# Kernel tuning notes

Hardware: AMD Instinct MI355X
Metric: run time of the kernel (lower is better)

The kernel has to match this reference:

```python
import jax, jax.numpy as jnp
import numpy as np

N = 100000       # nodes
E = 3200000      # edges (avg degree 32)
IN = 64          # in_channels
HID = 32         # hidden_channels
HEADS = 2
OUT = 1
EPS = 1e-5       # LayerNorm eps
SLOPE = 0.2      # LeakyReLU negative slope (PyG default)


def setup_inputs() -> dict:
    key = jax.random.key(0)
    ks = jax.random.split(key, 18)
    def nrm(k, shape, scale=0.1):
        return jax.random.normal(k, shape, dtype=jnp.float32) * scale
    return {
        "x": jax.random.normal(ks[0], (N, IN), dtype=jnp.float32),
        "edge_index": jax.random.randint(ks[1], (2, E), 0, N, dtype=jnp.int64),
        # GATConv layer 1 (concat=True)
        "W1": nrm(ks[2], (IN, HEADS * HID)),
        "a_src1": nrm(ks[3], (HEADS, HID)),
        "a_dst1": nrm(ks[4], (HEADS, HID)),
        "b1": jnp.zeros((HEADS * HID,), jnp.float32),
        "ln1_g": jnp.ones((HEADS * HID,), jnp.float32),
        "ln1_b": jnp.zeros((HEADS * HID,), jnp.float32),
        # GATConv layer 2 (heads=1, concat=False)
        "W2": nrm(ks[5], (HEADS * HID, HID)),
        "a_src2": nrm(ks[6], (1, HID)),
        "a_dst2": nrm(ks[7], (1, HID)),
        "b2": jnp.zeros((HID,), jnp.float32),
        "ln2_g": jnp.ones((HID,), jnp.float32),
        "ln2_b": jnp.zeros((HID,), jnp.float32),
        # output Linear
        "Wout": nrm(ks[8], (HID, OUT)),
        "bout": jnp.zeros((OUT,), jnp.float32),
    }


def layer_norm(x, g, b):
    mu = jnp.mean(x, axis=-1, keepdims=True)
    var = jnp.mean(jnp.square(x - mu), axis=-1, keepdims=True)
    return (x - mu) * jax.lax.rsqrt(var + EPS) * g + b


def gat_conv(x, edge_index, W, a_src, a_dst, bias, heads, ch, concat):
    """PyG GATConv (add_self_loops=True, bias=True), eval mode (no dropout)."""
    n = x.shape[0]
    loop = jnp.arange(n, dtype=edge_index.dtype)
    src = jnp.concatenate([edge_index[0], loop])   # [E+N]
    dst = jnp.concatenate([edge_index[1], loop])   # [E+N]
    h = (x @ W).reshape(n, heads, ch)              # [N,H,C]
    al_src = jnp.sum(h * a_src, axis=-1)           # [N,H]
    al_dst = jnp.sum(h * a_dst, axis=-1)           # [N,H]
    logits = jax.nn.leaky_relu(al_src[src] + al_dst[dst], SLOPE)  # [E+N,H]
    # segment softmax over destination nodes
    m = jax.lax.stop_gradient(jax.ops.segment_max(logits, dst, num_segments=n))
    e = jnp.exp(logits - m[dst])
    denom = jax.ops.segment_sum(e, dst, num_segments=n)
    alpha = e / denom[dst]                         # [E+N,H]
    out = jax.ops.segment_sum(h[src] * alpha[:, :, None], dst, num_segments=n)  # [N,H,C]
    out = out.reshape(n, heads * ch) if concat else out.mean(axis=1)
    return out + bias


def reference(x, edge_index, W1, a_src1, a_dst1, b1, ln1_g, ln1_b,
              W2, a_src2, a_dst2, b2, ln2_g, ln2_b, Wout, bout):
    h = gat_conv(x, edge_index, W1, a_src1, a_dst1, b1, HEADS, HID, True)
    h = jax.nn.elu(layer_norm(h, ln1_g, ln1_b))
    h = gat_conv(h, edge_index, W2, a_src2, a_dst2, b2, 1, HID, False)
    h = jax.nn.elu(layer_norm(h, ln2_g, ln2_b))
    return h @ Wout + bout  # [N, OUT]
```

## Files before the change

### kernel.cpp

```cpp
#include <hip/hip_runtime.h>

#define EPS 1e-5f
#define SLOPE 0.2f
#define MAXK 512
#define SEGCAP 12288
#define PBATCH 8192
#define AG1_SLOTS 8

__device__ __forceinline__ float leaky(float z) {
    return fmaxf(z, 0.f) + SLOPE * fminf(z, 0.f);
}
__device__ __forceinline__ ushort f2bf(float f) {
    unsigned u = __float_as_uint(f);
    u += 0x7FFFu + ((u >> 16) & 1u);
    return (ushort)(u >> 16);
}
__device__ __forceinline__ float bf2f(ushort b) {
    return __uint_as_float(((unsigned)b) << 16);
}
__device__ __forceinline__ float blo(unsigned u) {
    return __uint_as_float(u << 16);
}
__device__ __forceinline__ float bhi(unsigned u) {
    return __uint_as_float(u & 0xffff0000u);
}
__device__ __forceinline__ void gather16_to_lds(const void* g, void* l) {
    __builtin_amdgcn_global_load_lds(
        (const __attribute__((address_space(1))) void*)g,
        (__attribute__((address_space(3))) void*)l, 16, 0, 0);
}

__global__ __launch_bounds__(1024) void fused1(
    const int* __restrict__ ei, int E, int K, int* __restrict__ segcnt,
    unsigned* __restrict__ part,
    const float* __restrict__ x, const float* __restrict__ W1,
    const float* __restrict__ as1, const float* __restrict__ ad1,
    ushort* __restrict__ h1b, float* __restrict__ al_s, float* __restrict__ al_d,
    int N, int EB) {
    __shared__ float smem[4096 + 64 * 68];
    int t = threadIdx.x;
    if ((int)blockIdx.x < EB) {
        int* h   = (int*)smem;
        int* gp  = h + 512;
        int* run = h + 1024;
        for (int i = t; i < K; i += 1024) { h[i] = 0; run[i] = 0; }
        __syncthreads();
        int base = blockIdx.x * PBATCH;
        int sv[PBATCH / 1024], dv[PBATCH / 1024];
#pragma unroll
        for (int j = 0; j < PBATCH / 1024; j++) {
            int e = base + j * 1024 + t;
            sv[j] = (e < E) ? ei[e] : -1;
            dv[j] = (e < E) ? ei[E + e] : -1;
            if (dv[j] >= 0) atomicAdd(&h[dv[j] >> 8], 1);
        }
        __syncthreads();
        for (int i = t; i < K; i += 1024)
            gp[i] = h[i] ? atomicAdd(&segcnt[i * 16], h[i]) : 0;
        __syncthreads();
#pragma unroll
        for (int j = 0; j < PBATCH / 1024; j++) {
            if (dv[j] >= 0) {
                int b = dv[j] >> 8;
                int p = atomicAdd(&run[b], 1) + gp[b];
                if (p < SEGCAP)
                    part[(size_t)b * SEGCAP + p] =
                        ((unsigned)sv[j] << 8) | (unsigned)(dv[j] & 255);
            }
        }
        return;
    }
    float* Ws = smem;
    float (*xs)[68] = (float(*)[68])(smem + 4096);
    for (int i = t; i < 4096; i += 1024) Ws[i] = W1[i];
    int base = (blockIdx.x - EB) * 64;
    {
        int rr = t >> 4, kk = t & 15;
        int gr = base + rr;
        float4 vx = (gr < N) ? ((const float4*)x)[(size_t)gr * 16 + kk]
                             : make_float4(0.f, 0.f, 0.f, 0.f);
        *(float4*)&xs[rr][kk * 4] = vx;
    }
    __syncthreads();
    int wv = t >> 6, c = t & 63;
    int r0 = base + wv * 4;
    float acc0 = 0.f, acc1 = 0.f, acc2 = 0.f, acc3 = 0.f;
#pragma unroll
    for (int k = 0; k < 64; k += 4) {
        float4 x0 = *(const float4*)&xs[wv * 4 + 0][k];
        float4 x1 = *(const float4*)&xs[wv * 4 + 1][k];
        float4 x2 = *(const float4*)&xs[wv * 4 + 2][k];
        float4 x3 = *(const float4*)&xs[wv * 4 + 3][k];
        float w0 = Ws[(k + 0) * 64 + c];
        float w1 = Ws[(k + 1) * 64 + c];
        float w2 = Ws[(k + 2) * 64 + c];
        float w3 = Ws[(k + 3) * 64 + c];
        acc0 = fmaf(x0.x, w0, acc0); acc1 = fmaf(x1.x, w0, acc1);
        acc2 = fmaf(x2.x, w0, acc2); acc3 = fmaf(x3.x, w0, acc3);
        acc0 = fmaf(x0.y, w1, acc0); acc1 = fmaf(x1.y, w1, acc1);
        acc2 = fmaf(x2.y, w1, acc2); acc3 = fmaf(x3.y, w1, acc3);
        acc0 = fmaf(x0.z, w2, acc0); acc1 = fmaf(x1.z, w2, acc1);
        acc2 = fmaf(x2.z, w2, acc2); acc3 = fmaf(x3.z, w2, acc3);
        acc0 = fmaf(x0.w, w3, acc0); acc1 = fmaf(x1.w, w3, acc1);
        acc2 = fmaf(x2.w, w3, acc2); acc3 = fmaf(x3.w, w3, acc3);
    }
    int head = c >> 5, cc = c & 31;
    float asc = as1[head * 32 + cc], adc = ad1[head * 32 + cc];
    float vs0 = acc0 * asc, vd0 = acc0 * adc;
    float vs1 = acc1 * asc, vd1 = acc1 * adc;
    float vs2 = acc2 * asc, vd2 = acc2 * adc;
    float vs3 = acc3 * asc, vd3 = acc3 * adc;
#pragma unroll
    for (int off = 1; off < 32; off <<= 1) {
        vs0 += __shfl_xor(vs0, off); vd0 += __shfl_xor(vd0, off);
        vs1 += __shfl_xor(vs1, off); vd1 += __shfl_xor(vd1, off);
        vs2 += __shfl_xor(vs2, off); vd2 += __shfl_xor(vd2, off);
        vs3 += __shfl_xor(vs3, off); vd3 += __shfl_xor(vd3, off);
    }
    if (r0 + 0 < N) h1b[(size_t)(r0 + 0) * 64 + c] = f2bf(acc0);
    if (r0 + 1 < N) h1b[(size_t)(r0 + 1) * 64 + c] = f2bf(acc1);
    if (r0 + 2 < N) h1b[(size_t)(r0 + 2) * 64 + c] = f2bf(acc2);
    if (r0 + 3 < N) h1b[(size_t)(r0 + 3) * 64 + c] = f2bf(acc3);
    if (cc == 0) {
        if (r0 + 0 < N) { al_s[(r0 + 0) * 2 + head] = vs0; al_d[(r0 + 0) * 2 + head] = vd0; }
        if (r0 + 1 < N) { al_s[(r0 + 1) * 2 + head] = vs1; al_d[(r0 + 1) * 2 + head] = vd1; }
        if (r0 + 2 < N) { al_s[(r0 + 2) * 2 + head] = vs2; al_d[(r0 + 2) * 2 + head] = vd2; }
        if (r0 + 3 < N) { al_s[(r0 + 3) * 2 + head] = vs3; al_d[(r0 + 3) * 2 + head] = vd3; }
    }
}

__global__ __launch_bounds__(1024) void sortseg(
    const int* __restrict__ segcnt, int N,
    unsigned* __restrict__ part, int* __restrict__ nodeofs, int* __restrict__ cnt,
    int* __restrict__ perm) {
    __shared__ int h2[4096];
    __shared__ int sc[256];
    __shared__ int ex[256];
    __shared__ unsigned outb[SEGCAP];
    int b = blockIdx.x, t = threadIdx.x;
    size_t base = (size_t)b * SEGCAP;
    int sz = min(segcnt[b * 16], SEGCAP);
    for (int i = t; i < 4096; i += 1024) h2[i] = 0;
    __syncthreads();
    for (int i = t; i < sz; i += 1024) {
        unsigned code = part[base + i];
        int key = ((code & 255) << 4) | ((code >> 21) & 15);
        atomicAdd(&h2[key], 1);
    }
    __syncthreads();
    int v = 0;
    if (t < 256) {
#pragma unroll
        for (int i = 0; i < 16; i++) v += h2[t * 16 + i];
        sc[t] = v;
    }
    __syncthreads();
    for (int off = 1; off < 256; off <<= 1) {
        int xv = (t < 256 && t >= off) ? sc[t - off] : 0;
        __syncthreads();
        if (t < 256) sc[t] += xv;
        __syncthreads();
    }
    if (t < 256) {
        int exv = sc[t] - v;
        int run = exv;
#pragma unroll
        for (int i = 0; i < 16; i++) {
            int lc = h2[t * 16 + i];
            h2[t * 16 + i] = run;
            run += lc;
        }
        int n = b * 256 + t;
        if (n < N) { cnt[n] = v; nodeofs[n] = (int)(base + exv); }
    }
    __syncthreads();
    for (int i = t; i < sz; i += 1024) {
        unsigned code = part[base + i];
        int key = ((code & 255) << 4) | ((code >> 21) & 15);
        int p = atomicAdd(&h2[key], 1);
        outb[p] = code >> 8;
    }
    __syncthreads();
    for (int i = t; i < sz; i += 1024) part[base + i] = outb[i];
    __syncthreads();
    if (t < 256) h2[t] = 0;
    __syncthreads();
    int n = b * 256 + t;
    int dbin = min(v, 255);
    if (t < 256 && n < N) atomicAdd(&h2[dbin], 1);
    __syncthreads();
    int hv = (t < 256) ? h2[t] : 0;
    if (t < 256) sc[t] = hv;
    __syncthreads();
    for (int off = 1; off < 256; off <<= 1) {
        int xv = (t < 256 && t >= off) ? sc[t - off] : 0;
        __syncthreads();
        if (t < 256) sc[t] += xv;
        __syncthreads();
    }
    if (t < 256) ex[t] = sc[t] - hv;
    __syncthreads();
    if (t < 256 && n < N) {
        int r = atomicAdd(&ex[dbin], 1);
        perm[b * 256 + r] = n;
    }
}

__global__ __launch_bounds__(256) void aggB1(
    const ushort* __restrict__ h1b, const float* __restrict__ als,
    const float* __restrict__ ald, const int* __restrict__ nodeofs,
    const int* __restrict__ cnt, const unsigned* __restrict__ csr,
    const int* __restrict__ perm,
    const float* __restrict__ b1, const float* __restrict__ g1,
    const float* __restrict__ bb1, ushort* __restrict__ h1out, int N) {
    __shared__ uint4 stage[4][AG1_SLOTS * 64];
    int t = threadIdx.x;
    int wid = t >> 6, lane = t & 63;
    int grp = lane >> 3, q = lane & 7;
    int gbase = grp << 3;
    uint4* mystage = stage[wid];
    int idx = blockIdx.x * 32 + wid * 8 + grp;
    bool valid = idx < N;
    int nc = perm[min(idx, N - 1)];
    int head = q >> 2;
    const float2* als2 = (const float2*)als;
    const float2* ald2 = (const float2*)ald;
    float2 adv = ald2[nc], asv = als2[nc];
    float ad0 = adv.x, ad1v = adv.y;
    float wsf = __expf(leaky((head ? asv.y : asv.x) + (head ? ad1v : ad0)));
    const uint4* h4 = (const uint4*)h1b;
    uint4 hs = h4[(size_t)nc * 8 + q];
    float a0 = wsf * blo(hs.x), a1 = wsf * bhi(hs.x);
    float a2 = wsf * blo(hs.y), a3 = wsf * bhi(hs.y);
    float a4 = wsf * blo(hs.z), a5 = wsf * bhi(hs.z);
    float a6 = wsf * blo(hs.w), a7 = wsf * bhi(hs.w);
    float lp0 = 0.f, lp1 = 0.f;
    int ofs = valid ? nodeofs[nc] : 0;
    int deg = valid ? cnt[nc] : 0;
    int degm1 = max(deg - 1, 0);
    int degmax = deg;
    degmax = max(degmax, __shfl_xor(degmax, 8));
    degmax = max(degmax, __shfl_xor(degmax, 16));
    degmax = max(degmax, __shfl_xor(degmax, 32));
    int sq = 0;
    if (degmax > 0) sq = min((int)csr[ofs + min(q, degm1)], N - 1);
    for (int eb = 0; eb < degmax; eb += AG1_SLOTS) {
#pragma unroll
        for (int k = 0; k < AG1_SLOTS; k++) {
            int s = __shfl(sq, gbase + k);
            gather16_to_lds(h4 + ((size_t)s * 8 + q), &mystage[k * 64]);
        }
        float2 av = als2[sq];
        int nsq = sq;
        int ebn = eb + AG1_SLOTS;
        if (ebn < degmax)
            nsq = min((int)csr[ofs + min(ebn + q, degm1)], N - 1);
        bool ev = (eb + q < deg);
        float w0 = ev ? __expf(leaky(av.x + ad0)) : 0.f;
        float w1 = ev ? __expf(leaky(av.y + ad1v)) : 0.f;
        lp0 += w0;
        lp1 += w1;
        asm volatile("s_waitcnt vmcnt(0)" ::: "memory");
        __builtin_amdgcn_sched_barrier(0);
#pragma unroll
        for (int k = 0; k < AG1_SLOTS; k++) {
            float wk0 = __shfl(w0, gbase + k);
            float wk1 = __shfl(w1, gbase + k);
            float w = head ? wk1 : wk0;
            uint4 hv = mystage[k * 64 + lane];
            a0 = fmaf(w, blo(hv.x), a0); a1 = fmaf(w, bhi(hv.x), a1);
            a2 = fmaf(w, blo(hv.y), a2); a3 = fmaf(w, bhi(hv.y), a3);
            a4 = fmaf(w, blo(hv.z), a4); a5 = fmaf(w, bhi(hv.z), a5);
            a6 = fmaf(w, blo(hv.w), a6); a7 = fmaf(w, bhi(hv.w), a7);
        }
        sq = nsq;
    }
#pragma unroll
    for (int off = 1; off < 8; off <<= 1) {
        lp0 += __shfl_xor(lp0, off);
        lp1 += __shfl_xor(lp1, off);
    }
    if (!valid) return;
    float l = (head ? lp1 : lp0) + wsf;
    float inv = 1.f / l;
    float4 bA = ((const float4*)b1)[2 * q];
    float4 bB = ((const float4*)b1)[2 * q + 1];
    float v0 = a0 * inv + bA.x, v1 = a1 * inv + bA.y;
    float v2 = a2 * inv + bA.z, v3 = a3 * inv + bA.w;
    float v4 = a4 * inv + bB.x, v5 = a5 * inv + bB.y;
    float v6 = a6 * inv + bB.z, v7 = a7 * inv + bB.w;
    float s1 = v0 + v1 + v2 + v3 + v4 + v5 + v6 + v7;
#pragma unroll
    for (int off = 1; off < 8; off <<= 1) s1 += __shfl_xor(s1, off);
    float mu = s1 * (1.f / 64.f);
    float d0 = v0 - mu, d1 = v1 - mu, d2 = v2 - mu, d3 = v3 - mu;
    float d4 = v4 - mu, d5 = v5 - mu, d6 = v6 - mu, d7 = v7 - mu;
    float s2v = d0 * d0 + d1 * d1 + d2 * d2 + d3 * d3
              + d4 * d4 + d5 * d5 + d6 * d6 + d7 * d7;
#pragma unroll
    for (int off = 1; off < 8; off <<= 1) s2v += __shfl_xor(s2v, off);
    float rs = rsqrtf(s2v * (1.f / 64.f) + EPS);
    float4 gA = ((const float4*)g1)[2 * q];
    float4 gB = ((const float4*)g1)[2 * q + 1];
    float4 cA = ((const float4*)bb1)[2 * q];
    float4 cB = ((const float4*)bb1)[2 * q + 1];
    float y0 = d0 * rs * gA.x + cA.x;
    float y1 = d1 * rs * gA.y + cA.y;
    float y2 = d2 * rs * gA.z + cA.z;
    float y3 = d3 * rs * gA.w + cA.w;
    float y4 = d4 * rs * gB.x + cB.x;
    float y5 = d5 * rs * gB.y + cB.y;
    float y6 = d6 * rs * gB.z + cB.z;
    float y7 = d7 * rs * gB.w + cB.w;
    y0 = (y0 > 0.f) ? y0 : (__expf(y0) - 1.f);
    y1 = (y1 > 0.f) ? y1 : (__expf(y1) - 1.f);
    y2 = (y2 > 0.f) ? y2 : (__expf(y2) - 1.f);
    y3 = (y3 > 0.f) ? y3 : (__expf(y3) - 1.f);
    y4 = (y4 > 0.f) ? y4 : (__expf(y4) - 1.f);
    y5 = (y5 > 0.f) ? y5 : (__expf(y5) - 1.f);
    y6 = (y6 > 0.f) ? y6 : (__expf(y6) - 1.f);
    y7 = (y7 > 0.f) ? y7 : (__expf(y7) - 1.f);
    uint4 ov;
    ov.x = (unsigned)f2bf(y0) | ((unsigned)f2bf(y1) << 16);
    ov.y = (unsigned)f2bf(y2) | ((unsigned)f2bf(y3) << 16);
    ov.z = (unsigned)f2bf(y4) | ((unsigned)f2bf(y5) << 16);
    ov.w = (unsigned)f2bf(y6) | ((unsigned)f2bf(y7) << 16);
    ((uint4*)h1out)[(size_t)nc * 8 + q] = ov;
}

__global__ __launch_bounds__(256) void prep2(
    const ushort* __restrict__ h1ob, const float* __restrict__ W2,
    const float* __restrict__ as2, const float* __restrict__ ad2,
    ushort* __restrict__ h2b, float* __restrict__ al_s, float* __restrict__ al_d, int N) {
    __shared__ float Ws[64 * 32];
    __shared__ float xs[32][68];
    int t = threadIdx.x;
    for (int i = t; i < 64 * 32; i += 256) Ws[i] = W2[i];
    int base = blockIdx.x * 32;
    const ushort4* hv4 = (const ushort4*)h1ob;
    for (int i = t; i < 512; i += 256) {
        int rr = i >> 4, kk = i & 15;
        int gr = base + rr;
        ushort4 u = (gr < N) ? hv4[(unsigned)gr * 16 + kk] : make_ushort4(0, 0, 0, 0);
        xs[rr][kk * 4 + 0] = bf2f(u.x);
        xs[rr][kk * 4 + 1] = bf2f(u.y);
        xs[rr][kk * 4 + 2] = bf2f(u.z);
        xs[rr][kk * 4 + 3] = bf2f(u.w);
    }
    __syncthreads();
    int wv = t >> 6;
    int lane = t & 63;
    int half = lane >> 5, c = lane & 31;
    int rbase = wv * 8 + half * 4;
    int r0 = base + rbase;
    float acc0 = 0.f, acc1 = 0.f, acc2 = 0.f, acc3 = 0.f;
#pragma unroll
    for (int k = 0; k < 64; k += 4) {
        float4 x0 = *(const float4*)&xs[rbase + 0][k];
        float4 x1 = *(const float4*)&xs[rbase + 1][k];
        float4 x2 = *(const float4*)&xs[rbase + 2][k];
        float4 x3 = *(const float4*)&xs[rbase + 3][k];
        float w0 = Ws[(k + 0) * 32 + c];
        float w1 = Ws[(k + 1) * 32 + c];
        float w2 = Ws[(k + 2) * 32 + c];
        float w3 = Ws[(k + 3) * 32 + c];
        acc0 = fmaf(x0.x, w0, acc0); acc1 = fmaf(x1.x, w0, acc1);
        acc2 = fmaf(x2.x, w0, acc2); acc3 = fmaf(x3.x, w0, acc3);
        acc0 = fmaf(x0.y, w1, acc0); acc1 = fmaf(x1.y, w1, acc1);
        acc2 = fmaf(x2.y, w1, acc2); acc3 = fmaf(x3.y, w1, acc3);
        acc0 = fmaf(x0.z, w2, acc0); acc1 = fmaf(x1.z, w2, acc1);
        acc2 = fmaf(x2.z, w2, acc2); acc3 = fmaf(x3.z, w2, acc3);
        acc0 = fmaf(x0.w, w3, acc0); acc1 = fmaf(x1.w, w3, acc1);
        acc2 = fmaf(x2.w, w3, acc2); acc3 = fmaf(x3.w, w3, acc3);
    }
    float asc = as2[c], adc = ad2[c];
    float vs0 = acc0 * asc, vd0 = acc0 * adc;
    float vs1 = acc1 * asc, vd1 = acc1 * adc;
    float vs2 = acc2 * asc, vd2 = acc2 * adc;
    float vs3 = acc3 * asc, vd3 = acc3 * adc;
#pragma unroll
    for (int off = 1; off < 32; off <<= 1) {
        vs0 += __shfl_xor(vs0, off); vd0 += __shfl_xor(vd0, off);
        vs1 += __shfl_xor(vs1, off); vd1 += __shfl_xor(vd1, off);
        vs2 += __shfl_xor(vs2, off); vd2 += __shfl_xor(vd2, off);
        vs3 += __shfl_xor(vs3, off); vd3 += __shfl_xor(vd3, off);
    }
    if (r0 + 0 < N) h2b[(size_t)(r0 + 0) * 32 + c] = f2bf(acc0);
    if (r0 + 1 < N) h2b[(size_t)(r0 + 1) * 32 + c] = f2bf(acc1);
    if (r0 + 2 < N) h2b[(size_t)(r0 + 2) * 32 + c] = f2bf(acc2);
    if (r0 + 3 < N) h2b[(size_t)(r0 + 3) * 32 + c] = f2bf(acc3);
    if (c == 0) {
        if (r0 + 0 < N) { al_s[r0 + 0] = vs0; al_d[r0 + 0] = vd0; }
        if (r0 + 1 < N) { al_s[r0 + 1] = vs1; al_d[r0 + 1] = vd1; }
        if (r0 + 2 < N) { al_s[r0 + 2] = vs2; al_d[r0 + 2] = vd2; }
        if (r0 + 3 < N) { al_s[r0 + 3] = vs3; al_d[r0 + 3] = vd3; }
    }
}

__global__ __launch_bounds__(256, 2) void aggB2(
    const ushort* __restrict__ h2b, const float* __restrict__ als,
    const float* __restrict__ ald, const int* __restrict__ nodeofs,
    const int* __restrict__ cnt, const unsigned* __restrict__ csr,
    const int* __restrict__ perm,
    const float* __restrict__ b2, const float* __restrict__ g2,
    const float* __restrict__ bb2, const float* __restrict__ Wout,
    const float* __restrict__ bout, float* __restrict__ out, int N) {
    int lane = threadIdx.x & 63;
    int grp = lane >> 3, q = lane & 7;
    int gbase = grp << 3;
    int idx = blockIdx.x * 32 + (threadIdx.x >> 6) * 8 + grp;
    bool valid = idx < N;
    int nc = perm[min(idx, N - 1)];
    float myad = ald[nc];
    float wsf = __expf(leaky(als[nc] + myad));
    const ushort4* h4 = (const ushort4*)h2b;
    ushort4 hs = h4[(unsigned)nc * 8 + q];
    float a0 = wsf * bf2f(hs.x), a1 = wsf * bf2f(hs.y);
    float a2 = wsf * bf2f(hs.z), a3 = wsf * bf2f(hs.w);
    float lp = 0.f;
    int ofs = valid ? nodeofs[nc] : 0;
    int deg = valid ? cnt[nc] : 0;
    int degm1 = max(deg - 1, 0);
    int degmax = deg;
    degmax = max(degmax, __shfl_xor(degmax, 8));
    degmax = max(degmax, __shfl_xor(degmax, 16));
    degmax = max(degmax, __shfl_xor(degmax, 32));
    int sq0 = 0, sq1 = 0;
    if (degmax > 0) {
        int j0 = ofs + min(q, degm1);
        int j1 = ofs + min(8 + q, degm1);
        sq0 = min((int)csr[j0], N - 1);
        sq1 = min((int)csr[j1], N - 1);
    }
    for (int eb = 0; eb < degmax; eb += 16) {
        int s0[8], s1[8];
#pragma unroll
        for (int jj = 0; jj < 8; jj++) {
            s0[jj] = __shfl(sq0, gbase + jj);
            s1[jj] = __shfl(sq1, gbase + jj);
        }
        float av0 = als[sq0];
        float av1 = als[sq1];
        int nsq0 = sq0, nsq1 = sq1;
        int ebn = eb + 16;
        if (ebn < degmax) {
            int j0 = ofs + min(ebn + q, degm1);
            int j1 = ofs + min(ebn + 8 + q, degm1);
            nsq0 = min((int)csr[j0], N - 1);
            nsq1 = min((int)csr[j1], N - 1);
        }
        ushort4 r0[8], r1[8];
#pragma unroll
        for (int jj = 0; jj < 8; jj++) {
            r0[jj] = h4[(unsigned)s0[jj] * 8 + q];
            r1[jj] = h4[(unsigned)s1[jj] * 8 + q];
        }
        float z0 = leaky(av0 + myad);
        float z1 = leaky(av1 + myad);
        float wq0 = (eb + q < deg) ? __expf(z0) : 0.f;
        float wq1 = (eb + 8 + q < deg) ? __expf(z1) : 0.f;
        lp += wq0 + wq1;
        float w0a[8], w1a[8];
#pragma unroll
        for (int jj = 0; jj < 8; jj++) {
            w0a[jj] = __shfl(wq0, gbase + jj);
            w1a[jj] = __shfl(wq1, gbase + jj);
        }
#pragma unroll
        for (int jj = 0; jj < 8; jj++) {
            float w0 = w0a[jj], w1 = w1a[jj];
            a0 = fmaf(w0, bf2f(r0[jj].x), a0);
            a1 = fmaf(w0, bf2f(r0[jj].y), a1);
            a2 = fmaf(w0, bf2f(r0[jj].z), a2);
            a3 = fmaf(w0, bf2f(r0[jj].w), a3);
            a0 = fmaf(w1, bf2f(r1[jj].x), a0);
            a1 = fmaf(w1, bf2f(r1[jj].y), a1);
            a2 = fmaf(w1, bf2f(r1[jj].z), a2);
            a3 = fmaf(w1, bf2f(r1[jj].w), a3);
        }
        sq0 = nsq0;
        sq1 = nsq1;
    }
#pragma unroll
    for (int off = 1; off < 8; off <<= 1) lp += __shfl_xor(lp, off);
    if (!valid) return;
    float l = lp + wsf;
    float inv = 1.f / l;
    float4 bv = ((const float4*)b2)[q];
    float v0 = a0 * inv + bv.x, v1 = a1 * inv + bv.y;
    float v2 = a2 * inv + bv.z, v3 = a3 * inv + bv.w;
    float s1 = v0 + v1 + v2 + v3;
#pragma unroll
    for (int off = 1; off < 8; off <<= 1) s1 += __shfl_xor(s1, off);
    float mu = s1 * (1.f / 32.f);
    float d0 = v0 - mu, d1 = v1 - mu, d2 = v2 - mu, d3 = v3 - mu;
    float s2v = d0 * d0 + d1 * d1 + d2 * d2 + d3 * d3;
#pragma unroll
    for (int off = 1; off < 8; off <<= 1) s2v += __shfl_xor(s2v, off);
    float rs = rsqrtf(s2v * (1.f / 32.f) + EPS);
    float4 gv = ((const float4*)g2)[q];
    float4 bbv = ((const float4*)bb2)[q];
    float y0 = d0 * rs * gv.x + bbv.x;
    float y1 = d1 * rs * gv.y + bbv.y;
    float y2 = d2 * rs * gv.z + bbv.z;
    float y3 = d3 * rs * gv.w + bbv.w;
    y0 = (y0 > 0.f) ? y0 : (__expf(y0) - 1.f);
    y1 = (y1 > 0.f) ? y1 : (__expf(y1) - 1.f);
    y2 = (y2 > 0.f) ? y2 : (__expf(y2) - 1.f);
    y3 = (y3 > 0.f) ? y3 : (__expf(y3) - 1.f);
    float4 wo = ((const float4*)Wout)[q];
    float p = y0 * wo.x + y1 * wo.y + y2 * wo.z + y3 * wo.w;
#pragma unroll
    for (int off = 1; off < 8; off <<= 1) p += __shfl_xor(p, off);
    if (q == 0) out[nc] = p + bout[0];
}

extern "C" void kernel_launch(void* const* d_in, const int* in_sizes, int n_in,
                              void* d_out, int out_size, void* d_ws, size_t ws_size,
                              hipStream_t stream) {
    const float* x    = (const float*)d_in[0];
    const int*   ei   = (const int*)d_in[1];
    const float* W1   = (const float*)d_in[2];
    const float* as1  = (const float*)d_in[3];
    const float* ad1  = (const float*)d_in[4];
    const float* b1   = (const float*)d_in[5];
    const float* g1   = (const float*)d_in[6];
    const float* bb1  = (const float*)d_in[7];
    const float* W2   = (const float*)d_in[8];
    const float* as2  = (const float*)d_in[9];
    const float* ad2  = (const float*)d_in[10];
    const float* b2   = (const float*)d_in[11];
    const float* g2   = (const float*)d_in[12];
    const float* bb2  = (const float*)d_in[13];
    const float* Wout = (const float*)d_in[14];
    const float* bout = (const float*)d_in[15];
    float* out = (float*)d_out;

    const int N = in_sizes[0] / 64;
    const int E = in_sizes[1] / 2;
    const int K = (N + 255) / 256;

    auto align_up = [](size_t v) { return (v + 255) & ~(size_t)255; };
    char* ws = (char*)d_ws;
    unsigned* part    = (unsigned*)ws; ws += align_up((size_t)K * SEGCAP * 4);
    int*      segcnt  = (int*)ws;      ws += align_up((size_t)MAXK * 16 * 4);
    int*      nodeofs = (int*)ws;      ws += align_up((size_t)N * 4);
    int*      cnt     = (int*)ws;      ws += align_up((size_t)N * 4);
    int*      perm    = (int*)ws;      ws += align_up((size_t)(K * 256) * 4);
    ushort*   h1b     = (ushort*)ws;   ws += align_up((size_t)N * 64 * 2);
    ushort*   h1ob    = (ushort*)ws;   ws += align_up((size_t)N * 64 * 2);
    ushort*   h2b     = (ushort*)ws;   ws += align_up((size_t)N * 32 * 2);
    float*    al1s    = (float*)ws;    ws += align_up((size_t)N * 2 * 4);
    float*    al1d    = (float*)ws;    ws += align_up((size_t)N * 2 * 4);
    float*    al2s    = (float*)ws;    ws += align_up((size_t)N * 4);
    float*    al2d    = (float*)ws;    ws += align_up((size_t)N * 4);

    const int EB = (E + PBATCH - 1) / PBATCH;
    const int PB = (N + 63) / 64;

    hipMemsetAsync(segcnt, 0, (size_t)K * 16 * 4, stream);
    fused1<<<EB + PB, 1024, 0, stream>>>(ei, E, K, segcnt, part,
                                         x, W1, as1, ad1, h1b, al1s, al1d, N, EB);
    sortseg<<<K, 1024, 0, stream>>>(segcnt, N, part, nodeofs, cnt, perm);
    aggB1<<<(N + 31) / 32, 256, 0, stream>>>(h1b, al1s, al1d, nodeofs, cnt, part,
                                             perm, b1, g1, bb1, h1ob, N);
    prep2<<<(N + 31) / 32, 256, 0, stream>>>(h1ob, W2, as2, ad2, h2b, al2s, al2d, N);
    aggB2<<<(N + 31) / 32, 256, 0, stream>>>(h2b, al2s, al2d, nodeofs, cnt, part,
                                             perm, b2, g2, bb2, Wout, bout, out, N);
}
```

Baseline: 312.2 us.

## Fuse layer-2 linear projection and attention logits into aggB1 epilogue

Removes the prep2 kernel and the bf16 h1 output buffer by computing h1·W2 directly in the aggB1 epilogue. Each 8-lane group exchanges its post-ELU activations via shuffles and multiplies them against W2 staged in shared memory. The same epilogue also produces the layer-2 source/destination attention scalars. This saves a kernel launch plus a full write and read of the N×64 intermediate, and drops one bf16 rounding. In exchange aggB1 gains 8 KB of LDS, a block-wide W2 load and sync, and 64 shuffles plus 256 FMAs per lane, which may reduce occupancy.

Result: faster. 300.5 us (-3.8%).

```diff
diff --git a/kernel.cpp b/kernel.cpp
--- a/kernel.cpp
+++ b/kernel.cpp
@@ -212,9 +212,15 @@
     const int* __restrict__ cnt, const unsigned* __restrict__ csr,
     const int* __restrict__ perm,
     const float* __restrict__ b1, const float* __restrict__ g1,
-    const float* __restrict__ bb1, ushort* __restrict__ h1out, int N) {
+    const float* __restrict__ bb1,
+    const float* __restrict__ W2, const float* __restrict__ as2,
+    const float* __restrict__ ad2, ushort* __restrict__ h2b,
+    float* __restrict__ al2s, float* __restrict__ al2d, int N) {
     __shared__ uint4 stage[4][AG1_SLOTS * 64];
+    __shared__ float W2s[64 * 32];
     int t = threadIdx.x;
+    for (int i = t; i < 2048; i += 256) W2s[i] = W2[i];
+    __syncthreads();
     int wid = t >> 6, lane = t & 63;
     int grp = lane >> 3, q = lane & 7;
     int gbase = grp << 3;
@@ -304,97 +310,40 @@
     float4 gB = ((const float4*)g1)[2 * q + 1];
     float4 cA = ((const float4*)bb1)[2 * q];
     float4 cB = ((const float4*)bb1)[2 * q + 1];
-    float y0 = d0 * rs * gA.x + cA.x;
-    float y1 = d1 * rs * gA.y + cA.y;
-    float y2 = d2 * rs * gA.z + cA.z;
-    float y3 = d3 * rs * gA.w + cA.w;
-    float y4 = d4 * rs * gB.x + cB.x;
-    float y5 = d5 * rs * gB.y + cB.y;
-    float y6 = d6 * rs * gB.z + cB.z;
-    float y7 = d7 * rs * gB.w + cB.w;
-    y0 = (y0 > 0.f) ? y0 : (__expf(y0) - 1.f);
-    y1 = (y1 > 0.f) ? y1 : (__expf(y1) - 1.f);
-    y2 = (y2 > 0.f) ? y2 : (__expf(y2) - 1.f);
-    y3 = (y3 > 0.f) ? y3 : (__expf(y3) - 1.f);
-    y4 = (y4 > 0.f) ? y4 : (__expf(y4) - 1.f);
-    y5 = (y5 > 0.f) ? y5 : (__expf(y5) - 1.f);
-    y6 = (y6 > 0.f) ? y6 : (__expf(y6) - 1.f);
-    y7 = (y7 > 0.f) ? y7 : (__expf(y7) - 1.f);
-    uint4 ov;
-    ov.x = (unsigned)f2bf(y0) | ((unsigned)f2bf(y1) << 16);
-    ov.y = (unsigned)f2bf(y2) | ((unsigned)f2bf(y3) << 16);
-    ov.z = (unsigned)f2bf(y4) | ((unsigned)f2bf(y5) << 16);
-    ov.w = (unsigned)f2bf(y6) | ((unsigned)f2bf(y7) << 16);
-    ((uint4*)h1out)[(size_t)nc * 8 + q] = ov;
-}
-
-__global__ __launch_bounds__(256) void prep2(
-    const ushort* __restrict__ h1ob, const float* __restrict__ W2,
-    const float* __restrict__ as2, const float* __restrict__ ad2,
-    ushort* __restrict__ h2b, float* __restrict__ al_s, float* __restrict__ al_d, int N) {
-    __shared__ float Ws[64 * 32];
-    __shared__ float xs[32][68];
-    int t = threadIdx.x;
-    for (int i = t; i < 64 * 32; i += 256) Ws[i] = W2[i];
-    int base = blockIdx.x * 32;
-    const ushort4* hv4 = (const ushort4*)h1ob;
-    for (int i = t; i < 512; i += 256) {
-        int rr = i >> 4, kk = i & 15;
-        int gr = base + rr;
-        ushort4 u = (gr < N) ? hv4[(unsigned)gr * 16 + kk] : make_ushort4(0, 0, 0, 0);
-        xs[rr][kk * 4 + 0] = bf2f(u.x);
-        xs[rr][kk * 4 + 1] = bf2f(u.y);
-        xs[rr][kk * 4 + 2] = bf2f(u.z);
-        xs[rr][kk * 4 + 3] = bf2f(u.w);
-    }
-    __syncthreads();
-    int wv = t >> 6;
-    int lane = t & 63;
-    int half = lane >> 5, c = lane & 31;
-    int rbase = wv * 8 + half * 4;
-    int r0 = base + rbase;
-    float acc0 = 0.f, acc1 = 0.f, acc2 = 0.f, acc3 = 0.f;
-#pragma unroll
-    for (int k = 0; k < 64; k += 4) {
-        float4 x0 = *(const float4*)&xs[rbase + 0][k];
-        float4 x1 = *(const float4*)&xs[rbase + 1][k];
-        float4 x2 = *(const float4*)&xs[rbase + 2][k];
-        float4 x3 = *(const float4*)&xs[rbase + 3][k];
-        float w0 = Ws[(k + 0) * 32 + c];
-        float w1 = Ws[(k + 1) * 32 + c];
-        float w2 = Ws[(k + 2) * 32 + c];
-        float w3 = Ws[(k + 3) * 32 + c];
-        acc0 = fmaf(x0.x, w0, acc0); acc1 = fmaf(x1.x, w0, acc1);
-        acc2 = fmaf(x2.x, w0, acc2); acc3 = fmaf(x3.x, w0, acc3);
-        acc0 = fmaf(x0.y, w1, acc0); acc1 = fmaf(x1.y, w1, acc1);
-        acc2 = fmaf(x2.y, w1, acc2); acc3 = fmaf(x3.y, w1, acc3);
-        acc0 = fmaf(x0.z, w2, acc0); acc1 = fmaf(x1.z, w2, acc1);
-        acc2 = fmaf(x2.z, w2, acc2); acc3 = fmaf(x3.z, w2, acc3);
-        acc0 = fmaf(x0.w, w3, acc0); acc1 = fmaf(x1.w, w3, acc1);
-        acc2 = fmaf(x2.w, w3, acc2); acc3 = fmaf(x3.w, w3, acc3);
-    }
-    float asc = as2[c], adc = ad2[c];
-    float vs0 = acc0 * asc, vd0 = acc0 * adc;
-    float vs1 = acc1 * asc, vd1 = acc1 * adc;
-    float vs2 = acc2 * asc, vd2 = acc2 * adc;
-    float vs3 = acc3 * asc, vd3 = acc3 * adc;
-#pragma unroll
-    for (int off = 1; off < 32; off <<= 1) {
-        vs0 += __shfl_xor(vs0, off); vd0 += __shfl_xor(vd0, off);
-        vs1 += __shfl_xor(vs1, off); vd1 += __shfl_xor(vd1, off);
-        vs2 += __shfl_xor(vs2, off); vd2 += __shfl_xor(vd2, off);
-        vs3 += __shfl_xor(vs3, off); vd3 += __shfl_xor(vd3, off);
-    }
-    if (r0 + 0 < N) h2b[(size_t)(r0 + 0) * 32 + c] = f2bf(acc0);
-    if (r0 + 1 < N) h2b[(size_t)(r0 + 1) * 32 + c] = f2bf(acc1);
-    if (r0 + 2 < N) h2b[(size_t)(r0 + 2) * 32 + c] = f2bf(acc2);
-    if (r0 + 3 < N) h2b[(size_t)(r0 + 3) * 32 + c] = f2bf(acc3);
-    if (c == 0) {
-        if (r0 + 0 < N) { al_s[r0 + 0] = vs0; al_d[r0 + 0] = vd0; }
-        if (r0 + 1 < N) { al_s[r0 + 1] = vs1; al_d[r0 + 1] = vd1; }
-        if (r0 + 2 < N) { al_s[r0 + 2] = vs2; al_d[r0 + 2] = vd2; }
-        if (r0 + 3 < N) { al_s[r0 + 3] = vs3; al_d[r0 + 3] = vd3; }
-    }
+    float ya[8];
+    ya[0] = d0 * rs * gA.x + cA.x;
+    ya[1] = d1 * rs * gA.y + cA.y;
+    ya[2] = d2 * rs * gA.z + cA.z;
+    ya[3] = d3 * rs * gA.w + cA.w;
+    ya[4] = d4 * rs * gB.x + cB.x;
+    ya[5] = d5 * rs * gB.y + cB.y;
+    ya[6] = d6 * rs * gB.z + cB.z;
+    ya[7] = d7 * rs * gB.w + cB.w;
+#pragma unroll
+    for (int j = 0; j < 8; j++)
+        ya[j] = (ya[j] > 0.f) ? ya[j] : (__expf(ya[j]) - 1.f);
+    float o0 = 0.f, o1 = 0.f, o2 = 0.f, o3 = 0.f;
+#pragma unroll
+    for (int src = 0; src < 8; src++) {
+#pragma unroll
+        for (int j = 0; j < 8; j++) {
+            float yv = __shfl(ya[j], gbase + src);
+            float4 wr = *(const float4*)&W2s[(src * 8 + j) * 32 + 4 * q];
+            o0 = fmaf(yv, wr.x, o0);
+            o1 = fmaf(yv, wr.y, o1);
+            o2 = fmaf(yv, wr.z, o2);
+            o3 = fmaf(yv, wr.w, o3);
+        }
+    }
+    ((ushort4*)h2b)[(size_t)nc * 8 + q] =
+        make_ushort4(f2bf(o0), f2bf(o1), f2bf(o2), f2bf(o3));
+    float4 a2v = ((const float4*)as2)[q];
+    float4 d2v = ((const float4*)ad2)[q];
+    float ps = o0 * a2v.x + o1 * a2v.y + o2 * a2v.z + o3 * a2v.w;
+    float pd = o0 * d2v.x + o1 * d2v.y + o2 * d2v.z + o3 * d2v.w;
+    ps += __shfl_xor(ps, 1); ps += __shfl_xor(ps, 2); ps += __shfl_xor(ps, 4);
+    pd += __shfl_xor(pd, 1); pd += __shfl_xor(pd, 2); pd += __shfl_xor(pd, 4);
+    if (q == 0) { al2s[nc] = ps; al2d[nc] = pd; }
 }
 
 __global__ __launch_bounds__(256, 2) void aggB2(
@@ -548,7 +497,6 @@
     int*      cnt     = (int*)ws;      ws += align_up((size_t)N * 4);
     int*      perm    = (int*)ws;      ws += align_up((size_t)(K * 256) * 4);
     ushort*   h1b     = (ushort*)ws;   ws += align_up((size_t)N * 64 * 2);
-    ushort*   h1ob    = (ushort*)ws;   ws += align_up((size_t)N * 64 * 2);
     ushort*   h2b     = (ushort*)ws;   ws += align_up((size_t)N * 32 * 2);
     float*    al1s    = (float*)ws;    ws += align_up((size_t)N * 2 * 4);
     float*    al1d    = (float*)ws;    ws += align_up((size_t)N * 2 * 4);
@@ -563,8 +511,8 @@
                                          x, W1, as1, ad1, h1b, al1s, al1d, N, EB);
     sortseg<<<K, 1024, 0, stream>>>(segcnt, N, part, nodeofs, cnt, perm);
     aggB1<<<(N + 31) / 32, 256, 0, stream>>>(h1b, al1s, al1d, nodeofs, cnt, part,
-                                             perm, b1, g1, bb1, h1ob, N);
-    prep2<<<(N + 31) / 32, 256, 0, stream>>>(h1ob, W2, as2, ad2, h2b, al2s, al2d, N);
+                                             perm, b1, g1, bb1,
+                                             W2, as2, ad2, h2b, al2s, al2d, N);
     aggB2<<<(N + 31) / 32, 256, 0, stream>>>(h2b, al2s, al2d, nodeofs, cnt, part,
                                              perm, b2, g2, bb2, Wout, bout, out, N);
 }
```
